# Performance work log

Measured on AMD Instinct MI355X. Metric: run time of the kernel, lower is better.

Reference implementation:

```python
import jax, jax.numpy as jnp
import numpy as np


def setup_inputs() -> dict:
    key = jax.random.key(0)
    ks = jax.random.split(key, 6)
    B, L, D, H, U = 256, 225, 1280, 256, 256
    features = jax.random.normal(ks[0], (B, L, D), dtype=jnp.float32)
    hidden = jax.random.normal(ks[1], (B, H), dtype=jnp.float32)
    W1 = jax.random.normal(ks[2], (D, U), dtype=jnp.float32) * (1.0 / np.sqrt(D))
    b1 = jnp.zeros((U,), dtype=jnp.float32)
    W2 = jax.random.normal(ks[3], (H, U), dtype=jnp.float32) * (1.0 / np.sqrt(H))
    b2 = jnp.zeros((U,), dtype=jnp.float32)
    V = jax.random.normal(ks[4], (U, 1), dtype=jnp.float32) * (1.0 / np.sqrt(U))
    bV = jnp.zeros((1,), dtype=jnp.float32)
    return {"features": features, "hidden": hidden, "W1": W1, "b1": b1,
            "W2": W2, "b2": b2, "V": V, "bV": bV}


def reference(features, hidden, W1, b1, W2, b2, V, bV):
    # features: [B, L, D]; hidden: [B, H]
    proj_f = jnp.einsum('bld,du->blu', features, W1) + b1        # [B, L, U]
    proj_h = (hidden @ W2 + b2)[:, None, :]                      # [B, 1, U]
    score = jnp.tanh(proj_f + proj_h)                            # [B, L, U]
    logits = jnp.einsum('blu,uo->blo', score, V) + bV            # [B, L, 1]
    attn = jax.nn.softmax(logits, axis=1)                        # [B, L, 1]
    context = jnp.sum(attn * features, axis=1)                   # [B, D]
    return context
```

## Files before the change

### kernel.cpp

```cpp
#include <hip/hip_runtime.h>
#include <hip/hip_bf16.h>

#define B_ 256
#define L_ 1225
#undef L_
#define L_ 225
#define D_ 1280
#define H_ 256
#define U_ 256
#define LT 45
#define LTP 48

typedef __bf16  bf16x8 __attribute__((ext_vector_type(8)));
typedef float   f32x4  __attribute__((ext_vector_type(4)));
typedef unsigned short u16x8 __attribute__((ext_vector_type(8)));

__device__ __forceinline__ unsigned short f2bf(float f) {
    union { __hip_bfloat16 h; unsigned short u; } cv;
    cv.h = __float2bfloat16(f);
    return cv.u;
}

__device__ __forceinline__ void gload_lds16(const void* g, void* l) {
    __builtin_amdgcn_global_load_lds(
        (const __attribute__((address_space(1))) unsigned int*)g,
        (__attribute__((address_space(3))) unsigned int*)l,
        16, 0, 0);
}

__device__ __forceinline__ float wredsum(float x) {
#pragma unroll
    for (int off = 32; off > 0; off >>= 1) x += __shfl_xor(x, off, 64);
    return x;
}

__global__ void k_prep_w1t(const float* __restrict__ W1, __hip_bfloat16* __restrict__ w1t) {
    int idx = blockIdx.x * 256 + threadIdx.x;
    int k = idx / U_;
    int u = idx % U_;
    w1t[(size_t)u * D_ + k] = __float2bfloat16(W1[idx]);
}

__global__ void k_proj_h(const float* __restrict__ hidden, const float* __restrict__ W2,
                         const float* __restrict__ b1, const float* __restrict__ b2,
                         float* __restrict__ ph) {
    __shared__ float sh[H_];
    int b = blockIdx.x;
    int u = threadIdx.x;
    sh[u] = hidden[b * H_ + u];
    __syncthreads();
    float acc = b1[u] + b2[u];
#pragma unroll 8
    for (int h = 0; h < H_; ++h) acc += sh[h] * W2[h * U_ + u];
    ph[b * U_ + u] = acc;
}

__global__ __launch_bounds__(512, 4) void k_fused(
        const float* __restrict__ feat,
        const __hip_bfloat16* __restrict__ w1t,
        const float* __restrict__ ph,
        const float* __restrict__ Vv,
        float* __restrict__ num,
        float* __restrict__ den) {
    __shared__ __align__(128) char smem[79552];
    float* sL = (float*)(smem + 77824);
    float* sW = (float*)(smem + 79360);

    const int tid  = threadIdx.x;
    const int lane = tid & 63;
    const int wave = tid >> 6;
    const int blk  = blockIdx.x;
    const int b    = blk / 5;
    const int s5   = blk - b * 5;
    const int l0   = s5 * LT;

    const float* featB = feat + ((size_t)b * L_ + l0) * D_;

    const int ar   = tid >> 3;
    const int arc  = ar < LT ? ar : (LT - 1);
    const int ac8  = tid & 7;
    const bool aAct = (tid < 384);
    const float* aSrc0 = featB + (size_t)arc * D_ + ac8 * 8;
    const int aOff = ar * 128 + ((ac8 * 16) ^ ((ar & 7) << 4));

    const __hip_bfloat16* bSrc[4];
    int bDst[4];
#pragma unroll
    for (int pass = 0; pass < 4; ++pass) {
        int sI  = pass * 512 + tid;
        int u   = sI >> 3;
        int c8s = sI & 7;
        int c8g = c8s ^ (u & 7);
        bSrc[pass] = w1t + (size_t)u * D_ + c8g * 8;
        bDst[pass] = sI * 16;
    }

    f32x4 acc[3][2];
#pragma unroll
    for (int mi = 0; mi < 3; ++mi)
#pragma unroll
        for (int ni = 0; ni < 2; ++ni)
            acc[mi][ni] = (f32x4){0.f, 0.f, 0.f, 0.f};

    const int u0 = wave * 32 + (lane & 15);

    auto loadA = [&](int kt, f32x4* v) {
        if (aAct) {
            const float* src = aSrc0 + kt * 64;
            v[0] = *reinterpret_cast<const f32x4*>(src);
            v[1] = *reinterpret_cast<const f32x4*>(src + 4);
        }
    };
    auto storeA = [&](const f32x4* v, char* bufA) {
        if (aAct) {
            u16x8 w;
            w[0] = f2bf(v[0][0]); w[1] = f2bf(v[0][1]); w[2] = f2bf(v[0][2]); w[3] = f2bf(v[0][3]);
            w[4] = f2bf(v[1][0]); w[5] = f2bf(v[1][1]); w[6] = f2bf(v[1][2]); w[7] = f2bf(v[1][3]);
            *reinterpret_cast<u16x8*>(bufA + aOff) = w;
        }
    };
    auto stageB = [&](int kt, char* bufB) {
#pragma unroll
        for (int pass = 0; pass < 4; ++pass)
            gload_lds16(bSrc[pass] + kt * 64, bufB + bDst[pass]);
    };
    auto compute = [&](const char* bufA, const char* bufB) {
#pragma unroll
        for (int ks = 0; ks < 2; ++ks) {
            const int kk2 = (ks * 32 + ((lane >> 4) << 3)) * 2;
            bf16x8 a[3], bb[2];
#pragma unroll
            for (int mi = 0; mi < 3; ++mi) {
                int r = mi * 16 + (lane & 15);
                a[mi] = *reinterpret_cast<const bf16x8*>(
                    bufA + r * 128 + (kk2 ^ ((r & 7) << 4)));
            }
            bb[0] = *reinterpret_cast<const bf16x8*>(
                bufB + u0 * 128 + (kk2 ^ ((u0 & 7) << 4)));
            bb[1] = *reinterpret_cast<const bf16x8*>(
                bufB + (u0 + 16) * 128 + (kk2 ^ (((u0 + 16) & 7) << 4)));
#pragma unroll
            for (int mi = 0; mi < 3; ++mi)
#pragma unroll
                for (int ni = 0; ni < 2; ++ni)
                    acc[mi][ni] = __builtin_amdgcn_mfma_f32_16x16x32_bf16(
                        a[mi], bb[ni], acc[mi][ni], 0, 0, 0);
        }
    };

    {
        f32x4 v[2];
        loadA(0, v);
        stageB(0, smem + 12288);
        storeA(v, smem);
    }
    __syncthreads();
    int cur = 0;
    for (int kt = 0; kt < 20; ++kt) {
        f32x4 v[2];
        if (kt < 19) {
            loadA(kt + 1, v);
            stageB(kt + 1, smem + 12288 + (cur ^ 1) * 32768);
        }
        compute(smem + cur * 6144, smem + 12288 + cur * 32768);
        if (kt < 19) storeA(v, smem + (cur ^ 1) * 6144);
        __syncthreads();
        cur ^= 1;
    }

    const float* phB = ph + b * 256;
    float ph0 = phB[u0], ph1 = phB[u0 + 16];
    float v0  = Vv[u0],  v1  = Vv[u0 + 16];
#pragma unroll
    for (int mi = 0; mi < 3; ++mi) {
#pragma unroll
        for (int rg = 0; rg < 4; ++rg) {
            int row = mi * 16 + ((lane >> 4) << 2) + rg;
            float x0 = acc[mi][0][rg] + ph0;
            float x1 = acc[mi][1][rg] + ph1;
            float sl = (1.f - 2.f / (__expf(2.f * x0) + 1.f)) * v0
                     + (1.f - 2.f / (__expf(2.f * x1) + 1.f)) * v1;
            sl += __shfl_xor(sl, 1, 64);
            sl += __shfl_xor(sl, 2, 64);
            sl += __shfl_xor(sl, 4, 64);
            sl += __shfl_xor(sl, 8, 64);
            if ((lane & 15) == 0) sL[wave * LTP + row] = sl;
        }
    }
    __syncthreads();

    if (wave == 0) {
        float w = 0.f;
        if (lane < LT) {
            float lg = 0.f;
#pragma unroll
            for (int wc = 0; wc < 8; ++wc) lg += sL[wc * LTP + lane];
            w = __expf(lg);
            sW[lane] = w;
        }
        float d = wredsum(w);
        if (lane == 0) den[blk] = d;
    }
    __syncthreads();

    f32x4 c[5];
#pragma unroll
    for (int ch = 0; ch < 5; ++ch) c[ch] = (f32x4){0.f, 0.f, 0.f, 0.f};
    for (int l = wave; l < LT; l += 8) {
        float wgt = sW[l];
        const float* fr = featB + (size_t)l * D_ + (lane << 2);
#pragma unroll
        for (int ch = 0; ch < 5; ++ch)
            c[ch] += wgt * *reinterpret_cast<const f32x4*>(fr + ch * 256);
    }
    __syncthreads();

    float* pc = (float*)smem;
#pragma unroll
    for (int ch = 0; ch < 5; ++ch)
        *reinterpret_cast<f32x4*>(pc + wave * 1280 + ch * 256 + (lane << 2)) = c[ch];
    __syncthreads();
    if (tid < 320) {
        f32x4 s = (f32x4){0.f, 0.f, 0.f, 0.f};
#pragma unroll
        for (int w = 0; w < 8; ++w)
            s += *reinterpret_cast<const f32x4*>(pc + w * 1280 + (tid << 2));
        *reinterpret_cast<f32x4*>(num + (size_t)blk * 1280 + (tid << 2)) = s;
    }
}

__global__ void k_combine(const float* __restrict__ num, const float* __restrict__ den,
                          float* __restrict__ out) {
    int b = blockIdx.x;
    int t = threadIdx.x;
    f32x4 n = (f32x4){0.f, 0.f, 0.f, 0.f};
    float d = 0.f;
#pragma unroll
    for (int s = 0; s < 5; ++s) {
        n += *reinterpret_cast<const f32x4*>(num + (size_t)(b * 5 + s) * 1280 + (t << 2));
        d += den[b * 5 + s];
    }
    n *= (1.f / d);
    *reinterpret_cast<f32x4*>(out + (size_t)b * D_ + (t << 2)) = n;
}

extern "C" void kernel_launch(void* const* d_in, const int* in_sizes, int n_in,
                              void* d_out, int out_size, void* d_ws, size_t ws_size,
                              hipStream_t stream) {
    const float* feat   = (const float*)d_in[0];
    const float* hidden = (const float*)d_in[1];
    const float* W1     = (const float*)d_in[2];
    const float* b1     = (const float*)d_in[3];
    const float* W2     = (const float*)d_in[4];
    const float* b2     = (const float*)d_in[5];
    const float* Vv     = (const float*)d_in[6];

    char* ws = (char*)d_ws;
    __hip_bfloat16* w1t = (__hip_bfloat16*)(ws);
    float* ph  = (float*)(ws + 655360);
    float* num = (float*)(ws + 917504);
    float* den = (float*)(ws + 7471104);
    float* out = (float*)d_out;

    k_prep_w1t<<<(U_ * D_) / 256, 256, 0, stream>>>(W1, w1t);
    k_proj_h  <<<B_, U_, 0, stream>>>(hidden, W2, b1, b2, ph);
    k_fused   <<<B_ * 5, 512, 0, stream>>>(feat, w1t, ph, Vv, num, den);
    k_combine <<<B_, 320, 0, stream>>>(num, den, out);
}
```

Baseline: 152.9 us.

## Keep bf16 feature tiles in registers to avoid second feature pass; merge prep kernels

Each thread now loads and holds the bf16 version of its slice of the feature tile across all K steps, so the weighted context sum is computed from registers instead of re-reading the fp32 features from global memory. The A-tile staging is reorganized so that each thread owns 3 rows and 4 columns, with half the threads handling alternate k-steps. The W1 transpose and hidden projection kernels are merged into one launch. Costs: many more registers held live (30 u16x4 vectors), which may hurt occupancy or spill. The context sum now uses bf16-rounded features, so precision drops.

```diff
diff --git a/kernel.cpp b/kernel.cpp
--- a/kernel.cpp
+++ b/kernel.cpp
@@ -2,8 +2,6 @@
 #include <hip/hip_bf16.h>
 
 #define B_ 256
-#define L_ 1225
-#undef L_
 #define L_ 225
 #define D_ 1280
 #define H_ 256
@@ -14,11 +12,19 @@
 typedef __bf16  bf16x8 __attribute__((ext_vector_type(8)));
 typedef float   f32x4  __attribute__((ext_vector_type(4)));
 typedef unsigned short u16x8 __attribute__((ext_vector_type(8)));
+typedef unsigned short u16x4 __attribute__((ext_vector_type(4)));
 
 __device__ __forceinline__ unsigned short f2bf(float f) {
     union { __hip_bfloat16 h; unsigned short u; } cv;
     cv.h = __float2bfloat16(f);
     return cv.u;
+}
+
+__device__ __forceinline__ f32x4 bf4_to_f32(u16x4 w) {
+    union { unsigned u; float f; } a0, a1, a2, a3;
+    a0.u = (unsigned)w[0] << 16; a1.u = (unsigned)w[1] << 16;
+    a2.u = (unsigned)w[2] << 16; a3.u = (unsigned)w[3] << 16;
+    return (f32x4){a0.f, a1.f, a2.f, a3.f};
 }
 
 __device__ __forceinline__ void gload_lds16(const void* g, void* l) {
@@ -34,25 +40,30 @@
     return x;
 }
 
-__global__ void k_prep_w1t(const float* __restrict__ W1, __hip_bfloat16* __restrict__ w1t) {
-    int idx = blockIdx.x * 256 + threadIdx.x;
-    int k = idx / U_;
-    int u = idx % U_;
-    w1t[(size_t)u * D_ + k] = __float2bfloat16(W1[idx]);
-}
-
-__global__ void k_proj_h(const float* __restrict__ hidden, const float* __restrict__ W2,
-                         const float* __restrict__ b1, const float* __restrict__ b2,
-                         float* __restrict__ ph) {
-    __shared__ float sh[H_];
-    int b = blockIdx.x;
-    int u = threadIdx.x;
-    sh[u] = hidden[b * H_ + u];
-    __syncthreads();
-    float acc = b1[u] + b2[u];
+__global__ void k_prep(const float* __restrict__ W1,
+                       const float* __restrict__ hidden,
+                       const float* __restrict__ W2,
+                       const float* __restrict__ b1,
+                       const float* __restrict__ b2,
+                       __hip_bfloat16* __restrict__ w1t,
+                       float* __restrict__ ph) {
+    int bid = blockIdx.x;
+    if (bid < 1280) {
+        int idx = bid * 256 + threadIdx.x;
+        int k = idx / U_;
+        int u = idx % U_;
+        w1t[(size_t)u * D_ + k] = __float2bfloat16(W1[idx]);
+    } else {
+        __shared__ float sh[H_];
+        int b = bid - 1280;
+        int u = threadIdx.x;
+        sh[u] = hidden[b * H_ + u];
+        __syncthreads();
+        float acc = b1[u] + b2[u];
 #pragma unroll 8
-    for (int h = 0; h < H_; ++h) acc += sh[h] * W2[h * U_ + u];
-    ph[b * U_ + u] = acc;
+        for (int h = 0; h < H_; ++h) acc += sh[h] * W2[h * U_ + u];
+        ph[b * U_ + u] = acc;
+    }
 }
 
 __global__ __launch_bounds__(512, 4) void k_fused(
@@ -72,29 +83,34 @@
     const int blk  = blockIdx.x;
     const int b    = blk / 5;
     const int s5   = blk - b * 5;
-    const int l0   = s5 * LT;
-
-    const float* featB = feat + ((size_t)b * L_ + l0) * D_;
-
-    const int ar   = tid >> 3;
-    const int arc  = ar < LT ? ar : (LT - 1);
-    const int ac8  = tid & 7;
-    const bool aAct = (tid < 384);
-    const float* aSrc0 = featB + (size_t)arc * D_ + ac8 * 8;
-    const int aOff = ar * 128 + ((ac8 * 16) ^ ((ar & 7) << 4));
+
+    const float* featB = feat + ((size_t)b * L_ + s5 * LT) * D_;
+
+    const int g    = tid >> 5;
+    const int qw   = tid & 31;
+    const int half = qw >> 4;
+    const int ql   = qw & 15;
+
+    const float* aRow[3];
+    int aOff[3];
+#pragma unroll
+    for (int i = 0; i < 3; ++i) {
+        int r  = 3 * g + i;
+        int rc = r < LT ? r : (LT - 1);
+        aRow[i] = featB + (size_t)rc * D_ + ql * 4;
+        aOff[i] = r * 128 + ((ql * 8) ^ ((r & 7) << 4));
+    }
 
     const __hip_bfloat16* bSrc[4];
-    int bDst[4];
-#pragma unroll
-    for (int pass = 0; pass < 4; ++pass) {
-        int sI  = pass * 512 + tid;
-        int u   = sI >> 3;
-        int c8s = sI & 7;
-        int c8g = c8s ^ (u & 7);
-        bSrc[pass] = w1t + (size_t)u * D_ + c8g * 8;
-        bDst[pass] = sI * 16;
-    }
-
+#pragma unroll
+    for (int p = 0; p < 4; ++p) {
+        int sI = p * 512 + tid;
+        int u  = sI >> 3;
+        int c8 = (sI & 7) ^ (u & 7);
+        bSrc[p] = w1t + (size_t)u * D_ + c8 * 8;
+    }
+
+    u16x4 hold[10][3];
     f32x4 acc[3][2];
 #pragma unroll
     for (int mi = 0; mi < 3; ++mi)
@@ -104,27 +120,29 @@
 
     const int u0 = wave * 32 + (lane & 15);
 
-    auto loadA = [&](int kt, f32x4* v) {
-        if (aAct) {
-            const float* src = aSrc0 + kt * 64;
-            v[0] = *reinterpret_cast<const f32x4*>(src);
-            v[1] = *reinterpret_cast<const f32x4*>(src + 4);
-        }
+    auto stageB = [&](int s) {
+        char* bufB = smem + 12288 + (s & 1) * 32768;
+#pragma unroll
+        for (int p = 0; p < 4; ++p)
+            gload_lds16(bSrc[p] + s * 64, bufB + (p * 512 + tid) * 16);
     };
-    auto storeA = [&](const f32x4* v, char* bufA) {
-        if (aAct) {
-            u16x8 w;
-            w[0] = f2bf(v[0][0]); w[1] = f2bf(v[0][1]); w[2] = f2bf(v[0][2]); w[3] = f2bf(v[0][3]);
-            w[4] = f2bf(v[1][0]); w[5] = f2bf(v[1][1]); w[6] = f2bf(v[1][2]); w[7] = f2bf(v[1][3]);
-            *reinterpret_cast<u16x8*>(bufA + aOff) = w;
+    auto stageA = [&](int s) {
+        if ((s & 1) == half) {
+            char* bufA = smem + (s & 1) * 6144;
+#pragma unroll
+            for (int i = 0; i < 3; ++i) {
+                f32x4 v = *reinterpret_cast<const f32x4*>(aRow[i] + s * 64);
+                u16x4 q;
+                q[0] = f2bf(v[0]); q[1] = f2bf(v[1]);
+                q[2] = f2bf(v[2]); q[3] = f2bf(v[3]);
+                hold[s >> 1][i] = q;
+                *reinterpret_cast<u16x4*>(bufA + aOff[i]) = q;
+            }
         }
     };
-    auto stageB = [&](int kt, char* bufB) {
-#pragma unroll
-        for (int pass = 0; pass < 4; ++pass)
-            gload_lds16(bSrc[pass] + kt * 64, bufB + bDst[pass]);
-    };
-    auto compute = [&](const char* bufA, const char* bufB) {
+    auto compute = [&](int s) {
+        const char* bufA = smem + (s & 1) * 6144;
+        const char* bufB = smem + 12288 + (s & 1) * 32768;
 #pragma unroll
         for (int ks = 0; ks < 2; ++ks) {
             const int kk2 = (ks * 32 + ((lane >> 4) << 3)) * 2;
@@ -148,24 +166,14 @@
         }
     };
 
-    {
-        f32x4 v[2];
-        loadA(0, v);
-        stageB(0, smem + 12288);
-        storeA(v, smem);
-    }
-    __syncthreads();
-    int cur = 0;
-    for (int kt = 0; kt < 20; ++kt) {
-        f32x4 v[2];
-        if (kt < 19) {
-            loadA(kt + 1, v);
-            stageB(kt + 1, smem + 12288 + (cur ^ 1) * 32768);
-        }
-        compute(smem + cur * 6144, smem + 12288 + cur * 32768);
-        if (kt < 19) storeA(v, smem + (cur ^ 1) * 6144);
+    stageB(0);
+    stageA(0);
+    __syncthreads();
+#pragma unroll
+    for (int s = 0; s < 20; ++s) {
+        if (s < 19) { stageB(s + 1); stageA(s + 1); }
+        compute(s);
         __syncthreads();
-        cur ^= 1;
     }
 
     const float* phB = ph + b * 256;
@@ -198,33 +206,40 @@
             w = __expf(lg);
             sW[lane] = w;
         }
+        if (lane >= LT && lane < LTP) sW[lane] = 0.f;
         float d = wredsum(w);
         if (lane == 0) den[blk] = d;
     }
     __syncthreads();
 
-    f32x4 c[5];
-#pragma unroll
-    for (int ch = 0; ch < 5; ++ch) c[ch] = (f32x4){0.f, 0.f, 0.f, 0.f};
-    for (int l = wave; l < LT; l += 8) {
-        float wgt = sW[l];
-        const float* fr = featB + (size_t)l * D_ + (lane << 2);
-#pragma unroll
-        for (int ch = 0; ch < 5; ++ch)
-            c[ch] += wgt * *reinterpret_cast<const f32x4*>(fr + ch * 256);
-    }
-    __syncthreads();
-
     float* pc = (float*)smem;
-#pragma unroll
-    for (int ch = 0; ch < 5; ++ch)
-        *reinterpret_cast<f32x4*>(pc + wave * 1280 + ch * 256 + (lane << 2)) = c[ch];
+    const float w0 = sW[3 * g], w1 = sW[3 * g + 1], w2 = sW[3 * g + 2];
+    if (g < 8) {
+#pragma unroll
+        for (int w = 0; w < 10; ++w) {
+            f32x4 p = w0 * bf4_to_f32(hold[w][0])
+                    + w1 * bf4_to_f32(hold[w][1])
+                    + w2 * bf4_to_f32(hold[w][2]);
+            *reinterpret_cast<f32x4*>(pc + g * 1280 + w * 128 + qw * 4) = p;
+        }
+    }
+    __syncthreads();
+    if (g >= 8) {
+#pragma unroll
+        for (int w = 0; w < 10; ++w) {
+            f32x4 p = w0 * bf4_to_f32(hold[w][0])
+                    + w1 * bf4_to_f32(hold[w][1])
+                    + w2 * bf4_to_f32(hold[w][2]);
+            f32x4* dst = reinterpret_cast<f32x4*>(pc + (g - 8) * 1280 + w * 128 + qw * 4);
+            *dst += p;
+        }
+    }
     __syncthreads();
     if (tid < 320) {
         f32x4 s = (f32x4){0.f, 0.f, 0.f, 0.f};
 #pragma unroll
-        for (int w = 0; w < 8; ++w)
-            s += *reinterpret_cast<const f32x4*>(pc + w * 1280 + (tid << 2));
+        for (int j = 0; j < 8; ++j)
+            s += *reinterpret_cast<const f32x4*>(pc + j * 1280 + (tid << 2));
         *reinterpret_cast<f32x4*>(num + (size_t)blk * 1280 + (tid << 2)) = s;
     }
 }
@@ -262,8 +277,7 @@
     float* den = (float*)(ws + 7471104);
     float* out = (float*)d_out;
 
-    k_prep_w1t<<<(U_ * D_) / 256, 256, 0, stream>>>(W1, w1t);
-    k_proj_h  <<<B_, U_, 0, stream>>>(hidden, W2, b1, b2, ph);
-    k_fused   <<<B_ * 5, 512, 0, stream>>>(feat, w1t, ph, Vv, num, den);
-    k_combine <<<B_, 320, 0, stream>>>(num, den, out);
-}
+    k_prep   <<<1536, 256, 0, stream>>>(W1, hidden, W2, b1, b2, w1t, ph);
+    k_fused  <<<B_ * 5, 512, 0, stream>>>(feat, w1t, ph, Vv, num, den);
+    k_combine<<<B_, 320, 0, stream>>>(num, den, out);
+}
```

After: 225.8 us. 1.48x slower.
